# Kernel tuning notes

Measured on AMD Instinct MI355X. Metric: run time of the kernel, lower is better.

## Reference

```python
import jax, jax.numpy as jnp
import numpy as np

E_ENT = 50000   # entities
R_REL = 500     # relations (dual graph nodes)
N_EDGE = 500000 # triples
D = 256
HID = D // 2
ALPHA = 0.1
BETA = 0.3
SLOPE = 0.01    # torch F.leaky_relu default

def _leaky(x):
    return jnp.where(x > 0, x, SLOPE * x)

def _compute_r(X, head_r, tail_r):
    # mean head / tail entity embedding per relation -> [R, 2D]
    L = (head_r.T @ X) / head_r.sum(0)[:, None]
    Rm = (tail_r.T @ X) / tail_r.sum(0)[:, None]
    return jnp.concatenate([L, Rm], axis=-1)

def _dense_att(vals_in, feats, adj, w1, w2, b2, w3, b3):
    # conv1d(k=1) == linear; feats [R, 2D]
    in_fts = feats @ w1.T                # [R, HID]
    f1 = in_fts @ w2.T + b2              # [R, 1]
    f2 = in_fts @ w3.T + b3              # [R, 1]
    logits = adj * (f1 + f2.T)           # [R, R]
    bias = -1e9 * (1.0 - (adj > 0).astype(jnp.float32))
    coefs = jax.nn.softmax(_leaky(logits) + bias, axis=1)
    return jax.nn.relu(coefs @ vals_in)

def _sparse_att(X, dual_layer, row, col, rel, w, b):
    # per-relation scalar score, gathered per edge, sparse row-softmax, sparse mm
    score = (dual_layer @ w.T + b)[:, 0]          # [R]
    logit = _leaky(score[rel])                    # [E]
    m = jax.ops.segment_max(logit, row, num_segments=E_ENT)
    ex = jnp.exp(logit - m[row])
    s = jax.ops.segment_sum(ex, row, num_segments=E_ENT)
    coef = ex / s[row]
    out = jnp.zeros_like(X).at[row].add(coef[:, None] * X[col])
    return jax.nn.relu(out)

def _gcn(X, W, m_row, m_col, m_val):
    # sparse.mm(M, X * W); dropout omitted (eval mode)
    Xw = X * W
    out = jnp.zeros_like(X).at[m_row].add(m_val[:, None] * Xw[m_col])
    return jax.nn.relu(out)

def _highway(l1, l2, K, b):
    t = jax.nn.sigmoid(l1 @ K + b)
    return t * l2 + (1.0 - t) * l1

def setup_inputs() -> dict:
    key = jax.random.key(0)
    ks = jax.random.split(key, 24)
    e, r, ne, d, hid = E_ENT, R_REL, N_EDGE, D, HID
    u = lambda k, sh: jax.random.uniform(k, sh, dtype=jnp.float32)
    n = lambda k, sh: jax.random.normal(k, sh, dtype=jnp.float32)
    gl = lambda k, sh: n(k, sh) * (2.0 / (sh[0] + sh[-1])) ** 0.5
    return {
        'X0': n(ks[0], (e, d)) * 0.1,
        'head_r': u(ks[1], (e, r)),
        'tail_r': u(ks[2], (e, r)),
        'dual_A': u(ks[3], (r, r)),
        'edge_row': jax.random.randint(ks[4], (ne,), 0, e),
        'edge_col': jax.random.randint(ks[5], (ne,), 0, e),
        'edge_rel': jax.random.randint(ks[6], (ne,), 0, r),
        'm_row': jax.random.randint(ks[7], (ne,), 0, e),
        'm_col': jax.random.randint(ks[8], (ne,), 0, e),
        'm_val': u(ks[9], (ne,)) * 1e-1,
        'w_self1': gl(ks[10], (hid, 2 * d)),
        'w_self2': gl(ks[11], (1, hid)), 'b_self2': jnp.zeros((1,), jnp.float32),
        'w_self3': gl(ks[12], (1, hid)), 'b_self3': jnp.zeros((1,), jnp.float32),
        'w_sp1': gl(ks[13], (1, 2 * d)), 'b_sp1': jnp.zeros((1,), jnp.float32),
        'w_dual1': gl(ks[14], (hid, 2 * d)),
        'w_dual2': gl(ks[15], (1, hid)), 'b_dual2': jnp.zeros((1,), jnp.float32),
        'w_dual3': gl(ks[16], (1, hid)), 'b_dual3': jnp.zeros((1,), jnp.float32),
        'w_sp2': gl(ks[17], (1, 2 * d)), 'b_sp2': jnp.zeros((1,), jnp.float32),
        'w_gcn1': jnp.ones((1, d), jnp.float32),
        'w_gcn2': jnp.ones((1, d), jnp.float32),
        'k_hw1': gl(ks[18], (d, d)), 'bg_hw1': jnp.zeros((d,), jnp.float32),
        'k_hw2': gl(ks[19], (d, d)), 'bg_hw2': jnp.zeros((d,), jnp.float32),
    }

def reference(X0, head_r, tail_r, dual_A, edge_row, edge_col, edge_rel,
              m_row, m_col, m_val,
              w_self1, w_self2, b_self2, w_self3, b_self3, w_sp1, b_sp1,
              w_dual1, w_dual2, b_dual2, w_dual3, b_dual3, w_sp2, b_sp2,
              w_gcn1, w_gcn2, k_hw1, bg_hw1, k_hw2, bg_hw2):
    dX1 = _compute_r(X0, head_r, tail_r)
    dH1 = _dense_att(dX1, dX1, dual_A, w_self1, w_self2, b_self2, w_self3, b_self3)
    pH1 = _sparse_att(X0, dH1, edge_row, edge_col, edge_rel, w_sp1, b_sp1)
    pX1 = X0 + ALPHA * pH1
    dX2 = _compute_r(pX1, head_r, tail_r)
    dH2 = _dense_att(dH1, dX2, dual_A, w_dual1, w_dual2, b_dual2, w_dual3, b_dual3)
    pH2 = _sparse_att(pX1, dH2, edge_row, edge_col, edge_rel, w_sp2, b_sp2)
    pX2 = X0 + BETA * pH2
    g1 = _gcn(pX2, w_gcn1, m_row, m_col, m_val)
    h1 = _highway(pX2, g1, k_hw1, bg_hw1)
    g2 = _gcn(h1, w_gcn2, m_row, m_col, m_val)
    return _highway(h1, g2, k_hw2, bg_hw2)
```

## Files before the change

kernel.cpp:

```cpp
#include <hip/hip_runtime.h>
#include <stdint.h>

#define E_ENT 50000
#define R_REL 500
#define NEDGE 500000
#define DD 256
#define D2 512
#define KSPLIT 50
#define KCHUNK 1000

typedef unsigned short u16;
typedef unsigned int u32;
typedef __attribute__((ext_vector_type(8))) short bf16x8;
typedef __attribute__((ext_vector_type(4))) float f32x4;

__device__ __forceinline__ float bf2f(u16 u) {
  union { u32 i; float f; } v; v.i = ((u32)u) << 16; return v.f;
}
__device__ __forceinline__ u16 f2bf(float f) {
  union { float f; u32 i; } v; v.f = f;
  u32 r = v.i + 0x7fffu + ((v.i >> 16) & 1u);
  return (u16)(r >> 16);
}
__device__ __forceinline__ float lrelu(float x) { return x > 0.f ? x : 0.01f * x; }

__device__ __forceinline__ uint4 ld4g(const u16* p, bool v) {
  if (v) return *(const uint4*)p;
  return make_uint4(0u, 0u, 0u, 0u);
}

__device__ __forceinline__ int lds_addr(int col, int e) {
  return col * 64 + ((((e >> 3) ^ col ^ (col >> 3)) & 7) << 3) + (e & 7);
}

__device__ __forceinline__ void pack_store(u16* __restrict__ lds, int colBase, int e,
                                           const uint4& x, const uint4& y) {
  const u32* xp = (const u32*)&x;
  const u32* yp = (const u32*)&y;
#pragma unroll
  for (int i = 0; i < 4; ++i) {
    u32 xv = xp[i], yv = yp[i];
    u32 lo = (xv & 0xffffu) | (yv << 16);
    u32 hi = (xv >> 16) | (yv & 0xffff0000u);
    int c0 = colBase + 2 * i;
    *(u32*)(lds + lds_addr(c0, e)) = lo;
    *(u32*)(lds + lds_addr(c0 + 1, e)) = hi;
  }
}

__global__ void k_cast(const float* __restrict__ in, u16* __restrict__ out, int n4) {
  int i = blockIdx.x * 256 + threadIdx.x;
  if (i < n4) {
    float4 v = *(const float4*)(in + (size_t)i * 4);
    uint2 o;
    o.x = (u32)f2bf(v.x) | ((u32)f2bf(v.y) << 16);
    o.y = (u32)f2bf(v.z) | ((u32)f2bf(v.w) << 16);
    *(uint2*)(out + (size_t)i * 4) = o;
  }
}

__global__ __launch_bounds__(256) void k_castW(const float* __restrict__ W,
                                               u16* __restrict__ WB,
                                               float* __restrict__ sums) {
  int tid = threadIdx.x;
  int c0 = tid * 2;
  int r0 = blockIdx.x * 64;
  bool valid = c0 < R_REL;
  float s0 = 0.f, s1 = 0.f;
  for (int e = 0; e < 64; ++e) {
    int row = r0 + e;
    if (row >= E_ENT) break;
    u32 out = 0;
    if (valid) {
      float2 v = *(const float2*)(W + (size_t)row * R_REL + c0);
      s0 += v.x; s1 += v.y;
      out = (u32)f2bf(v.x) | ((u32)f2bf(v.y) << 16);
    }
    *(u32*)(WB + (size_t)row * D2 + c0) = out;
  }
  if (valid) {
    atomicAdd(&sums[c0], s0);
    atomicAdd(&sums[c0 + 1], s1);
  }
}

__global__ void k_hist(const int* __restrict__ rows, int* __restrict__ cnt) {
  int i = blockIdx.x * 256 + threadIdx.x;
  if (i < NEDGE) atomicAdd(&cnt[rows[i]], 1);
}

__global__ void k_bsum(const int* __restrict__ cnt, int* __restrict__ bsum) {
  __shared__ int sb[256];
  int t = threadIdx.x, i = blockIdx.x * 256 + t;
  sb[t] = (i < E_ENT) ? cnt[i] : 0;
  __syncthreads();
  for (int s = 128; s; s >>= 1) { if (t < s) sb[t] += sb[t + s]; __syncthreads(); }
  if (t == 0) bsum[blockIdx.x] = sb[0];
}

__global__ void k_scanb(const int* __restrict__ bsum, int* __restrict__ boff, int nb) {
  __shared__ int sb[256];
  int t = threadIdx.x;
  int v = (t < nb) ? bsum[t] : 0;
  sb[t] = v;
  __syncthreads();
  for (int o = 1; o < 256; o <<= 1) {
    int x = (t >= o) ? sb[t - o] : 0;
    __syncthreads();
    sb[t] += x;
    __syncthreads();
  }
  if (t < nb) boff[t] = sb[t] - v;
}

__global__ void k_apply(const int* __restrict__ cnt, const int* __restrict__ boff,
                        int* __restrict__ ptr, int* __restrict__ cur) {
  __shared__ int sb[256];
  int t = threadIdx.x, b = blockIdx.x, i = b * 256 + t;
  int v = (i < E_ENT) ? cnt[i] : 0;
  sb[t] = v;
  __syncthreads();
  for (int o = 1; o < 256; o <<= 1) {
    int x = (t >= o) ? sb[t - o] : 0;
    __syncthreads();
    sb[t] += x;
    __syncthreads();
  }
  if (i < E_ENT) { int ex = boff[b] + sb[t] - v; ptr[i] = ex; cur[i] = ex; }
  if (b == 0 && t == 0) ptr[E_ENT] = NEDGE;
}

__global__ void k_scat_e(const int* __restrict__ rows, const int* __restrict__ cols,
                         const int* __restrict__ rels, int* __restrict__ cur,
                         int* __restrict__ cs, int* __restrict__ rs) {
  int i = blockIdx.x * 256 + threadIdx.x;
  if (i < NEDGE) {
    int p = atomicAdd(&cur[rows[i]], 1);
    cs[p] = cols[i];
    rs[p] = rels[i];
  }
}

__global__ void k_scat_m(const int* __restrict__ rows, const int* __restrict__ cols,
                         const float* __restrict__ vals, int* __restrict__ cur,
                         int* __restrict__ cs, float* __restrict__ vs) {
  int i = blockIdx.x * 256 + threadIdx.x;
  if (i < NEDGE) {
    int p = atomicAdd(&cur[rows[i]], 1);
    cs[p] = cols[i];
    vs[p] = vals[i];
  }
}

__device__ __forceinline__ void wtx_load(const u16* __restrict__ WSel, const u16* __restrict__ XB,
                                         int eb, int e_end, int r0, int n0,
                                         int ap, int aq, int ep0, int ep1, int nq,
                                         uint4& a0, uint4& a1, uint4& b00, uint4& b01,
                                         uint4& b10, uint4& b11) {
  int ee = e_end - eb;
  const u16* p = WSel + (size_t)(eb + 2 * ap) * D2 + r0 + aq * 8;
  a0 = ld4g(p, 2 * ap < ee);
  a1 = ld4g(p + D2, 2 * ap + 1 < ee);
  const u16* q0 = XB + (size_t)(eb + 2 * ep0) * DD + n0 + nq * 8;
  b00 = ld4g(q0, 2 * ep0 < ee);
  b01 = ld4g(q0 + DD, 2 * ep0 + 1 < ee);
  const u16* q1 = XB + (size_t)(eb + 2 * ep1) * DD + n0 + nq * 8;
  b10 = ld4g(q1, 2 * ep1 < ee);
  b11 = ld4g(q1 + DD, 2 * ep1 + 1 < ee);
}

__global__ __launch_bounds__(256) void k_wtx(const u16* __restrict__ HB,
                                             const u16* __restrict__ TB,
                                             const u16* __restrict__ XB,
                                             float* __restrict__ P) {
  __shared__ __align__(16) u16 lsa2[2 * 32 * 64];
  __shared__ __align__(16) u16 lsb[128 * 64];
  const int tid = threadIdx.x;
  const int bid = blockIdx.x;
  const int swz = (bid & 7) * 200 + (bid >> 3);
  const int mtnt = swz & 31;
  const int mt = mtnt >> 1, nt = mtnt & 1;
  const int chunk = swz >> 5;
  const int r0 = mt * 32, n0 = nt * 128;
  const int lane = tid & 63, wv = tid >> 6;
  const int wm = (wv & 1) * 16, wn = (wv >> 1) * 64;
  const int l15 = lane & 15, lq = lane >> 4;
  const int ap = (tid & 127) >> 2, aq = tid & 3;
  const int ep0 = tid >> 4, nq = tid & 15;
  const int ep1 = ep0 + 16;
  const u16* WSel = (tid < 128) ? HB : TB;
  u16* lsaSel = lsa2 + (tid >> 7) * (32 * 64);
  const int e_begin = chunk * KCHUNK;
  const int e_end = min(e_begin + KCHUNK, E_ENT);
  const int iters = (e_end - e_begin + 63) >> 6;

  f32x4 accH[4], accT[4];
#pragma unroll
  for (int t = 0; t < 4; ++t) { accH[t] = (f32x4)0.f; accT[t] = (f32x4)0.f; }

  uint4 a0, a1, b00, b01, b10, b11;
  wtx_load(WSel, XB, e_begin, e_end, r0, n0, ap, aq, ep0, ep1, nq, a0, a1, b00, b01, b10, b11);

  int eb = e_begin;
  for (int it = 0; it < iters; ++it) {
    __syncthreads();
    pack_store(lsaSel, aq * 8, 2 * ap, a0, a1);
    pack_store(lsb, nq * 8, 2 * ep0, b00, b01);
    pack_store(lsb, nq * 8, 2 * ep1, b10, b11);
    __syncthreads();
    eb += 64;
    if (it + 1 < iters)
      wtx_load(WSel, XB, eb, e_end, r0, n0, ap, aq, ep0, ep1, nq, a0, a1, b00, b01, b10, b11);
#pragma unroll
    for (int ks = 0; ks < 2; ++ks) {
      bf16x8 afH = *(const bf16x8*)(lsa2 + lds_addr(wm + l15, ks * 32 + lq * 8));
      bf16x8 afT = *(const bf16x8*)(lsa2 + 32 * 64 + lds_addr(wm + l15, ks * 32 + lq * 8));
#pragma unroll
      for (int t = 0; t < 4; ++t) {
        bf16x8 bv = *(const bf16x8*)(lsb + lds_addr(wn + t * 16 + l15, ks * 32 + lq * 8));
        accH[t] = __builtin_amdgcn_mfma_f32_16x16x32_bf16(afH, bv, accH[t], 0, 0, 0);
        accT[t] = __builtin_amdgcn_mfma_f32_16x16x32_bf16(afT, bv, accT[t], 0, 0, 0);
      }
    }
  }
#pragma unroll
  for (int t = 0; t < 4; ++t) {
#pragma unroll
    for (int rg = 0; rg < 4; ++rg) {
      int row = r0 + wm + lq * 4 + rg;
      if (row < R_REL) {
        int col = n0 + wn + t * 16 + l15;
        atomicAdd(&P[row * D2 + col], accH[t][rg]);
        atomicAdd(&P[row * D2 + col + 256], accT[t][rg]);
      }
    }
  }
}

__global__ void k_fin(float* __restrict__ P, const float* __restrict__ hsum,
                      const float* __restrict__ tsum) {
  int i = blockIdx.x * 256 + threadIdx.x;
  if (i < R_REL * D2) {
    int r = i >> 9, c = i & 511;
    P[i] = P[i] / (c < 256 ? hsum[r] : tsum[r]);
  }
}

__global__ __launch_bounds__(128) void k_infts(const float* __restrict__ feats,
                                               const float* __restrict__ w1,
                                               const float* __restrict__ w2, const float* __restrict__ b2,
                                               const float* __restrict__ w3, const float* __restrict__ b3,
                                               float* __restrict__ f1, float* __restrict__ f2) {
  __shared__ float fl[512];
  __shared__ float red[128];
  int r = blockIdx.x, t = threadIdx.x;
  for (int i = t; i < 512; i += 128) fl[i] = feats[r * 512 + i];
  __syncthreads();
  float a = 0.f;
  const float* wrow = w1 + (size_t)t * 512;
  for (int k = 0; k < 512; k += 4) {
    float4 v = *(const float4*)(wrow + k);
    a += fl[k + 0] * v.x + fl[k + 1] * v.y + fl[k + 2] * v.z + fl[k + 3] * v.w;
  }
  red[t] = a * w2[t];
  __syncthreads();
  for (int s = 64; s; s >>= 1) { if (t < s) red[t] += red[t + s]; __syncthreads(); }
  if (t == 0) f1[r] = red[0] + b2[0];
  __syncthreads();
  red[t] = a * w3[t];
  __syncthreads();
  for (int s = 64; s; s >>= 1) { if (t < s) red[t] += red[t + s]; __syncthreads(); }
  if (t == 0) f2[r] = red[0] + b3[0];
}

__global__ __launch_bounds__(256) void k_att(const float* __restrict__ adj,
                                             const float* __restrict__ f1,
                                             const float* __restrict__ f2,
                                             const float* __restrict__ vals,
                                             float* __restrict__ dH) {
  __shared__ float coef[512];
  __shared__ float red[256];
  int r = blockIdx.x, t = threadIdx.x;
  float f1r = f1[r];
  float z0, z1 = -1e30f;
  {
    float a = adj[r * 500 + t];
    float z = lrelu(a * (f1r + f2[t]));
    if (!(a > 0.f)) z += -1e9f;
    z0 = z;
  }
  int c1 = t + 256;
  if (c1 < 500) {
    float a = adj[r * 500 + c1];
    float z = lrelu(a * (f1r + f2[c1]));
    if (!(a > 0.f)) z += -1e9f;
    z1 = z;
  }
  red[t] = fmaxf(z0, z1);
  __syncthreads();
  for (int s = 128; s; s >>= 1) { if (t < s) red[t] = fmaxf(red[t], red[t + s]); __syncthreads(); }
  float m = red[0];
  __syncthreads();
  float e0 = expf(z0 - m);
  float e1 = (c1 < 500) ? expf(z1 - m) : 0.f;
  coef[t] = e0;
  coef[c1] = e1;
  red[t] = e0 + e1;
  __syncthreads();
  for (int s = 128; s; s >>= 1) { if (t < s) red[t] += red[t + s]; __syncthreads(); }
  float inv = 1.f / red[0];
  float accA = 0.f, accB = 0.f;
  int dA = t, dB = t + 256;
  for (int c = 0; c < 500; ++c) {
    float cf = coef[c];
    accA += cf * vals[c * 512 + dA];
    accB += cf * vals[c * 512 + dB];
  }
  dH[r * 512 + dA] = fmaxf(accA * inv, 0.f);
  dH[r * 512 + dB] = fmaxf(accB * inv, 0.f);
}

__global__ void k_score(const float* __restrict__ dH, const float* __restrict__ w,
                        const float* __restrict__ b, float* __restrict__ score) {
  int r = blockIdx.x, lane = threadIdx.x;
  float a = 0.f;
  for (int k = lane; k < 512; k += 64) a += dH[r * 512 + k] * w[k];
  for (int o = 32; o; o >>= 1) a += __shfl_xor(a, o, 64);
  if (lane == 0) score[r] = a + b[0];
}

__global__ void k_els(const float* __restrict__ score, float* __restrict__ EL) {
  __shared__ float red[512];
  int t = threadIdx.x;
  float v = (t < R_REL) ? lrelu(score[t]) : -3.0e38f;
  red[t] = v;
  __syncthreads();
  for (int s = 256; s; s >>= 1) { if (t < s) red[t] = fmaxf(red[t], red[t + s]); __syncthreads(); }
  float m = red[0];
  EL[t] = (t < R_REL) ? expf(v - m) : 0.f;
}

__global__ __launch_bounds__(256) void k_spatt(const u16* __restrict__ src,
                                               const float* __restrict__ base,
                                               const int* __restrict__ ptr,
                                               const int* __restrict__ cols,
                                               const int* __restrict__ rels,
                                               const float* __restrict__ EL, float alpha,
                                               u16* __restrict__ outb, float* __restrict__ outf) {
  __shared__ float sEL[512];
  const int tid = threadIdx.x;
  sEL[tid] = EL[tid];
  sEL[tid + 256] = EL[tid + 256];
  __syncthreads();
  const int lane = tid & 63;
  const int e = blockIdx.x * 4 + (tid >> 6);
  int p0 = ptr[e], p1 = ptr[e + 1];
  float a0 = 0.f, a1 = 0.f, a2 = 0.f, a3 = 0.f;
  if (p1 > p0) {
    float s = 0.f;
    for (int j = p0 + lane; j < p1; j += 64) s += sEL[rels[j]];
    for (int o = 32; o; o >>= 1) s += __shfl_xor(s, o, 64);
    float inv = 1.f / s;
    for (int jb = p0; jb < p1; jb += 64) {
      int n = min(64, p1 - jb);
      int cl = 0; float wl = 0.f;
      if (lane < n) { cl = cols[jb + lane]; wl = sEL[rels[jb + lane]] * inv; }
      int jj = 0;
      for (; jj + 4 <= n; jj += 4) {
        int c0 = __shfl(cl, jj), c1 = __shfl(cl, jj + 1), c2 = __shfl(cl, jj + 2), c3 = __shfl(cl, jj + 3);
        float w0 = __shfl(wl, jj), w1 = __shfl(wl, jj + 1), w2 = __shfl(wl, jj + 2), w3 = __shfl(wl, jj + 3);
        uint2 v0 = *(const uint2*)(src + (size_t)c0 * DD + lane * 4);
        uint2 v1 = *(const uint2*)(src + (size_t)c1 * DD + lane * 4);
        uint2 v2 = *(const uint2*)(src + (size_t)c2 * DD + lane * 4);
        uint2 v3 = *(const uint2*)(src + (size_t)c3 * DD + lane * 4);
        a0 += w0 * bf2f((u16)(v0.x & 0xffffu)) + w1 * bf2f((u16)(v1.x & 0xffffu))
            + w2 * bf2f((u16)(v2.x & 0xffffu)) + w3 * bf2f((u16)(v3.x & 0xffffu));
        a1 += w0 * bf2f((u16)(v0.x >> 16)) + w1 * bf2f((u16)(v1.x >> 16))
            + w2 * bf2f((u16)(v2.x >> 16)) + w3 * bf2f((u16)(v3.x >> 16));
        a2 += w0 * bf2f((u16)(v0.y & 0xffffu)) + w1 * bf2f((u16)(v1.y & 0xffffu))
            + w2 * bf2f((u16)(v2.y & 0xffffu)) + w3 * bf2f((u16)(v3.y & 0xffffu));
        a3 += w0 * bf2f((u16)(v0.y >> 16)) + w1 * bf2f((u16)(v1.y >> 16))
            + w2 * bf2f((u16)(v2.y >> 16)) + w3 * bf2f((u16)(v3.y >> 16));
      }
      for (; jj < n; ++jj) {
        int c = __shfl(cl, jj);
        float w = __shfl(wl, jj);
        uint2 v = *(const uint2*)(src + (size_t)c * DD + lane * 4);
        a0 += w * bf2f((u16)(v.x & 0xffffu));
        a1 += w * bf2f((u16)(v.x >> 16));
        a2 += w * bf2f((u16)(v.y & 0xffffu));
        a3 += w * bf2f((u16)(v.y >> 16));
      }
    }
  }
  size_t off = (size_t)e * DD + lane * 4;
  float4 bv = *(const float4*)(base + off);
  float o0 = bv.x + alpha * fmaxf(a0, 0.f);
  float o1 = bv.y + alpha * fmaxf(a1, 0.f);
  float o2 = bv.z + alpha * fmaxf(a2, 0.f);
  float o3 = bv.w + alpha * fmaxf(a3, 0.f);
  uint2 ov;
  ov.x = (u32)f2bf(o0) | ((u32)f2bf(o1) << 16);
  ov.y = (u32)f2bf(o2) | ((u32)f2bf(o3) << 16);
  *(uint2*)(outb + off) = ov;
  if (outf) *(float4*)(outf + off) = make_float4(o0, o1, o2, o3);
}

__global__ __launch_bounds__(256) void k_gcn(const u16* __restrict__ src,
                                             const int* __restrict__ ptr,
                                             const int* __restrict__ cols,
                                             const float* __restrict__ vals,
                                             const float* __restrict__ wg,
                                             float* __restrict__ gout) {
  const int lane = threadIdx.x & 63;
  const int e = blockIdx.x * 4 + (threadIdx.x >> 6);
  int p0 = ptr[e], p1 = ptr[e + 1];
  float a0 = 0.f, a1 = 0.f, a2 = 0.f, a3 = 0.f;
  for (int jb = p0; jb < p1; jb += 64) {
    int n = min(64, p1 - jb);
    int cl = 0; float wl = 0.f;
    if (lane < n) { cl = cols[jb + lane]; wl = vals[jb + lane]; }
    int jj = 0;
    for (; jj + 4 <= n; jj += 4) {
      int c0 = __shfl(cl, jj), c1 = __shfl(cl, jj + 1), c2 = __shfl(cl, jj + 2), c3 = __shfl(cl, jj + 3);
      float w0 = __shfl(wl, jj), w1 = __shfl(wl, jj + 1), w2 = __shfl(wl, jj + 2), w3 = __shfl(wl, jj + 3);
      uint2 v0 = *(const uint2*)(src + (size_t)c0 * DD + lane * 4);
      uint2 v1 = *(const uint2*)(src + (size_t)c1 * DD + lane * 4);
      uint2 v2 = *(const uint2*)(src + (size_t)c2 * DD + lane * 4);
      uint2 v3 = *(const uint2*)(src + (size_t)c3 * DD + lane * 4);
      a0 += w0 * bf2f((u16)(v0.x & 0xffffu)) + w1 * bf2f((u16)(v1.x & 0xffffu))
          + w2 * bf2f((u16)(v2.x & 0xffffu)) + w3 * bf2f((u16)(v3.x & 0xffffu));
      a1 += w0 * bf2f((u16)(v0.x >> 16)) + w1 * bf2f((u16)(v1.x >> 16))
          + w2 * bf2f((u16)(v2.x >> 16)) + w3 * bf2f((u16)(v3.x >> 16));
      a2 += w0 * bf2f((u16)(v0.y & 0xffffu)) + w1 * bf2f((u16)(v1.y & 0xffffu))
          + w2 * bf2f((u16)(v2.y & 0xffffu)) + w3 * bf2f((u16)(v3.y & 0xffffu));
      a3 += w0 * bf2f((u16)(v0.y >> 16)) + w1 * bf2f((u16)(v1.y >> 16))
          + w2 * bf2f((u16)(v2.y >> 16)) + w3 * bf2f((u16)(v3.y >> 16));
    }
    for (; jj < n; ++jj) {
      int c = __shfl(cl, jj);
      float w = __shfl(wl, jj);
      uint2 v = *(const uint2*)(src + (size_t)c * DD + lane * 4);
      a0 += w * bf2f((u16)(v.x & 0xffffu));
      a1 += w * bf2f((u16)(v.x >> 16));
      a2 += w * bf2f((u16)(v.y & 0xffffu));
      a3 += w * bf2f((u16)(v.y >> 16));
    }
  }
  int d = lane * 4;
  float4 wv = *(const float4*)(wg + d);
  float4 o = make_float4(fmaxf(a0 * wv.x, 0.f), fmaxf(a1 * wv.y, 0.f),
                         fmaxf(a2 * wv.z, 0.f), fmaxf(a3 * wv.w, 0.f));
  *(float4*)(gout + (size_t)e * DD + d) = o;
}

__global__ __launch_bounds__(256) void k_hw(const u16* __restrict__ xb,
                                            const float* __restrict__ xf,
                                            const float* __restrict__ g,
                                            const u16* __restrict__ KB,
                                            const float* __restrict__ bg,
                                            float* __restrict__ outf,
                                            u16* __restrict__ outb) {
  __shared__ __align__(16) u16 la[64 * 64];
  __shared__ __align__(16) u16 lb[64 * 64];
  const int tid = threadIdx.x;
  const int bid = blockIdx.x;
  const int swz = (bid & 7) * 391 + (bid >> 3);
  const int e0 = (swz >> 2) * 64;
  const int n0 = (swz & 3) * 64;
  const int lane = tid & 63, wv = tid >> 6;
  const int m0 = wv * 16;
  const int l15 = lane & 15, lq = lane >> 4;
  const int am = tid >> 3, aoct = tid & 7;
  const int kp = tid >> 3, nq8 = tid & 7;
  f32x4 acc[4];
#pragma unroll
  for (int t = 0; t < 4; ++t) acc[t] = (f32x4)0.f;

  for (int kc = 0; kc < 4; ++kc) {
    {
      const u16* pa = xb + (size_t)(e0 + am) * DD + kc * 64 + aoct * 8;
      uint4 va = ld4g(pa, e0 + am < E_ENT);
      *(uint4*)(la + lds_addr(am, aoct * 8)) = va;
      const u16* pa2 = xb + (size_t)(e0 + am + 32) * DD + kc * 64 + aoct * 8;
      uint4 va2 = ld4g(pa2, e0 + am + 32 < E_ENT);
      *(uint4*)(la + lds_addr(am + 32, aoct * 8)) = va2;
      const u16* pb = KB + (size_t)(kc * 64 + 2 * kp) * DD + n0 + nq8 * 8;
      uint4 xk = *(const uint4*)pb;
      uint4 yk = *(const uint4*)(pb + DD);
      pack_store(lb, nq8 * 8, 2 * kp, xk, yk);
    }
    __syncthreads();
#pragma unroll
    for (int ks = 0; ks < 2; ++ks) {
      bf16x8 af = *(const bf16x8*)(la + lds_addr(m0 + l15, ks * 32 + lq * 8));
#pragma unroll
      for (int t = 0; t < 4; ++t) {
        bf16x8 bv = *(const bf16x8*)(lb + lds_addr(t * 16 + l15, ks * 32 + lq * 8));
        acc[t] = __builtin_amdgcn_mfma_f32_16x16x32_bf16(af, bv, acc[t], 0, 0, 0);
      }
    }
    __syncthreads();
  }
#pragma unroll
  for (int t = 0; t < 4; ++t) {
    int col = n0 + t * 16 + l15;
    float bgv = bg[col];
#pragma unroll
    for (int rg = 0; rg < 4; ++rg) {
      int row = e0 + m0 + lq * 4 + rg;
      if (row < E_ENT) {
        float z = acc[t][rg] + bgv;
        float tt = 1.f / (1.f + expf(-z));
        size_t off = (size_t)row * DD + col;
        float hv = tt * g[off] + (1.f - tt) * xf[off];
        outf[off] = hv;
        if (outb) outb[off] = f2bf(hv);
      }
    }
  }
}

extern "C" void kernel_launch(void* const* d_in, const int* in_sizes, int n_in,
                              void* d_out, int out_size, void* d_ws, size_t ws_size,
                              hipStream_t stream) {
  (void)in_sizes; (void)n_in; (void)out_size;
  const float* X0 = (const float*)d_in[0];
  const float* head = (const float*)d_in[1];
  const float* tail = (const float*)d_in[2];
  const float* adj = (const float*)d_in[3];
  const int* erow = (const int*)d_in[4];
  const int* ecol = (const int*)d_in[5];
  const int* erel = (const int*)d_in[6];
  const int* mrow = (const int*)d_in[7];
  const int* mcol = (const int*)d_in[8];
  const float* mval = (const float*)d_in[9];
  const float* w_self1 = (const float*)d_in[10];
  const float* w_self2 = (const float*)d_in[11];
  const float* b_self2 = (const float*)d_in[12];
  const float* w_self3 = (const float*)d_in[13];
  const float* b_self3 = (const float*)d_in[14];
  const float* w_sp1 = (const float*)d_in[15];
  const float* b_sp1 = (const float*)d_in[16];
  const float* w_dual1 = (const float*)d_in[17];
  const float* w_dual2 = (const float*)d_in[18];
  const float* b_dual2 = (const float*)d_in[19];
  const float* w_dual3 = (const float*)d_in[20];
  const float* b_dual3 = (const float*)d_in[21];
  const float* w_sp2 = (const float*)d_in[22];
  const float* b_sp2 = (const float*)d_in[23];
  const float* w_gcn1 = (const float*)d_in[24];
  const float* w_gcn2 = (const float*)d_in[25];
  const float* k_hw1 = (const float*)d_in[26];
  const float* bg_hw1 = (const float*)d_in[27];
  const float* k_hw2 = (const float*)d_in[28];
  const float* bg_hw2 = (const float*)d_in[29];

  char* ws = (char*)d_ws;
  size_t o = 0;
  auto take = [&](size_t bytes) -> char* {
    o = (o + 255) & ~(size_t)255;
    char* p = ws + o;
    o += bytes;
    return p;
  };
  u16* X0B  = (u16*)take((size_t)E_ENT * DD * 2);
  u16* PX1B = (u16*)take((size_t)E_ENT * DD * 2);
  u16* PX2B = (u16*)take((size_t)E_ENT * DD * 2);
  u16* H1B  = (u16*)take((size_t)E_ENT * DD * 2);
  float* PX2F = (float*)take((size_t)E_ENT * DD * 4);
  float* G    = (float*)take((size_t)E_ENT * DD * 4);
  float* P1   = (float*)take((size_t)512 * 512 * 4);
  float* P2   = (float*)take((size_t)512 * 512 * 4);
  float* DH1  = (float*)take((size_t)512 * 512 * 4);
  float* DH2  = (float*)take((size_t)512 * 512 * 4);
  float* HS   = (float*)take(1024 * 4);
  float* F1   = (float*)take(512 * 4);
  float* F2   = (float*)take(512 * 4);
  float* SCORE = (float*)take(512 * 4);
  float* EL   = (float*)take(512 * 4);
  u16* KB1 = (u16*)take((size_t)DD * DD * 2);
  u16* KB2 = (u16*)take((size_t)DD * DD * 2);
  int* BSUM = (int*)take(256 * 4);
  int* BOFF = (int*)take(256 * 4);
  int* EPTR = (int*)take((size_t)(E_ENT + 1) * 4);
  int* ECUR = (int*)take((size_t)(E_ENT + 1) * 4);
  int* ECOLS = (int*)take((size_t)NEDGE * 4);
  int* ERELS = (int*)take((size_t)NEDGE * 4);
  int* MPTR = (int*)take((size_t)(E_ENT + 1) * 4);
  int* MCUR = (int*)take((size_t)(E_ENT + 1) * 4);
  int* MCOLS = (int*)take((size_t)NEDGE * 4);
  float* MVALS = (float*)take((size_t)NEDGE * 4);

  u16* HB = (u16*)PX2F;
  u16* TB = (u16*)G;

  if (o > ws_size) {
    hipMemsetAsync(d_out, 0, (size_t)E_ENT * DD * 4, stream);
    return;
  }

  hipMemsetAsync(P1, 0, (size_t)512 * 512 * 4, stream);
  hipMemsetAsync(P2, 0, (size_t)512 * 512 * 4, stream);
  hipMemsetAsync(HS, 0, 1024 * 4, stream);
  hipMemsetAsync(ECUR, 0, (size_t)(E_ENT + 1) * 4, stream);
  hipMemsetAsync(MCUR, 0, (size_t)(E_ENT + 1) * 4, stream);

  const int GE = (NEDGE + 255) / 256;
  const int GB = (E_ENT + 255) / 256;
  const int GW = (E_ENT + 63) / 64;

  k_cast<<<(E_ENT * DD / 4 + 255) / 256, 256, 0, stream>>>(X0, X0B, E_ENT * DD / 4);
  k_cast<<<64, 256, 0, stream>>>(k_hw1, KB1, DD * DD / 4);
  k_cast<<<64, 256, 0, stream>>>(k_hw2, KB2, DD * DD / 4);
  k_castW<<<GW, 256, 0, stream>>>(head, HB, HS);
  k_castW<<<GW, 256, 0, stream>>>(tail, TB, HS + 512);

  k_hist<<<GE, 256, 0, stream>>>(erow, ECUR);
  k_bsum<<<GB, 256, 0, stream>>>(ECUR, BSUM);
  k_scanb<<<1, 256, 0, stream>>>(BSUM, BOFF, GB);
  k_apply<<<GB, 256, 0, stream>>>(ECUR, BOFF, EPTR, ECUR);
  k_scat_e<<<GE, 256, 0, stream>>>(erow, ecol, erel, ECUR, ECOLS, ERELS);
  k_hist<<<GE, 256, 0, stream>>>(mrow, MCUR);
  k_bsum<<<GB, 256, 0, stream>>>(MCUR, BSUM);
  k_scanb<<<1, 256, 0, stream>>>(BSUM, BOFF, GB);
  k_apply<<<GB, 256, 0, stream>>>(MCUR, BOFF, MPTR, MCUR);
  k_scat_m<<<GE, 256, 0, stream>>>(mrow, mcol, mval, MCUR, MCOLS, MVALS);

  k_wtx<<<32 * KSPLIT, 256, 0, stream>>>(HB, TB, X0B, P1);
  k_fin<<<1000, 256, 0, stream>>>(P1, HS, HS + 512);
  k_infts<<<500, 128, 0, stream>>>(P1, w_self1, w_self2, b_self2, w_self3, b_self3, F1, F2);
  k_att<<<500, 256, 0, stream>>>(adj, F1, F2, P1, DH1);
  k_score<<<500, 64, 0, stream>>>(DH1, w_sp1, b_sp1, SCORE);
  k_els<<<1, 512, 0, stream>>>(SCORE, EL);
  k_spatt<<<12500, 256, 0, stream>>>(X0B, X0, EPTR, ECOLS, ERELS, EL, 0.1f, PX1B, nullptr);

  k_wtx<<<32 * KSPLIT, 256, 0, stream>>>(HB, TB, PX1B, P2);
  k_fin<<<1000, 256, 0, stream>>>(P2, HS, HS + 512);
  k_infts<<<500, 128, 0, stream>>>(P2, w_dual1, w_dual2, b_dual2, w_dual3, b_dual3, F1, F2);
  k_att<<<500, 256, 0, stream>>>(adj, F1, F2, DH1, DH2);
  k_score<<<500, 64, 0, stream>>>(DH2, w_sp2, b_sp2, SCORE);
  k_els<<<1, 512, 0, stream>>>(SCORE, EL);
  k_spatt<<<12500, 256, 0, stream>>>(PX1B, X0, EPTR, ECOLS, ERELS, EL, 0.3f, PX2B, PX2F);

  k_gcn<<<12500, 256, 0, stream>>>(PX2B, MPTR, MCOLS, MVALS, w_gcn1, G);
  k_hw<<<782 * 4, 256, 0, stream>>>(PX2B, PX2F, G, KB1, bg_hw1, PX2F, H1B);
  k_gcn<<<12500, 256, 0, stream>>>(H1B, MPTR, MCOLS, MVALS, w_gcn2, G);
  k_hw<<<782 * 4, 256, 0, stream>>>(H1B, PX2F, G, KB2, bg_hw2, (float*)d_out, nullptr);
}
```

Baseline: 1.109 ms.

## Fuse head/tail fp32-to-bf16 cast and column sums into WtX GEMM loads

Drops the separate k_castW pre-pass that converted the head/tail incidence matrices to padded bf16 and summed their columns. k_wtx now loads fp32 rows directly, packs them to bf16 in registers before the LDS store, and on the first call also accumulates the per-relation column sums, reduced through LDS and then atomics. This removes a full read-write pass over two large matrices and two launches. The cost is that each GEMM call now reads fp32 data, twice the bytes of bf16, and each slice is fetched by both n-tiles, so total traffic may not shrink unless the cache absorbs the repeats.

```diff
diff --git a/kernel.cpp b/kernel.cpp
--- a/kernel.cpp
+++ b/kernel.cpp
@@ -27,6 +27,19 @@
 __device__ __forceinline__ uint4 ld4g(const u16* p, bool v) {
   if (v) return *(const uint4*)p;
   return make_uint4(0u, 0u, 0u, 0u);
+}
+__device__ __forceinline__ float4 ldf4(const float* p, bool v) {
+  if (v) return *(const float4*)p;
+  return make_float4(0.f, 0.f, 0.f, 0.f);
+}
+
+__device__ __forceinline__ uint4 pk4(const float4& x, const float4& y) {
+  uint4 r;
+  r.x = (u32)f2bf(x.x) | ((u32)f2bf(x.y) << 16);
+  r.y = (u32)f2bf(x.z) | ((u32)f2bf(x.w) << 16);
+  r.z = (u32)f2bf(y.x) | ((u32)f2bf(y.y) << 16);
+  r.w = (u32)f2bf(y.z) | ((u32)f2bf(y.w) << 16);
+  return r;
 }
 
 __device__ __forceinline__ int lds_addr(int col, int e) {
@@ -59,31 +72,6 @@
   }
 }
 
-__global__ __launch_bounds__(256) void k_castW(const float* __restrict__ W,
-                                               u16* __restrict__ WB,
-                                               float* __restrict__ sums) {
-  int tid = threadIdx.x;
-  int c0 = tid * 2;
-  int r0 = blockIdx.x * 64;
-  bool valid = c0 < R_REL;
-  float s0 = 0.f, s1 = 0.f;
-  for (int e = 0; e < 64; ++e) {
-    int row = r0 + e;
-    if (row >= E_ENT) break;
-    u32 out = 0;
-    if (valid) {
-      float2 v = *(const float2*)(W + (size_t)row * R_REL + c0);
-      s0 += v.x; s1 += v.y;
-      out = (u32)f2bf(v.x) | ((u32)f2bf(v.y) << 16);
-    }
-    *(u32*)(WB + (size_t)row * D2 + c0) = out;
-  }
-  if (valid) {
-    atomicAdd(&sums[c0], s0);
-    atomicAdd(&sums[c0 + 1], s1);
-  }
-}
-
 __global__ void k_hist(const int* __restrict__ rows, int* __restrict__ cnt) {
   int i = blockIdx.x * 256 + threadIdx.x;
   if (i < NEDGE) atomicAdd(&cnt[rows[i]], 1);
@@ -152,15 +140,20 @@
   }
 }
 
-__device__ __forceinline__ void wtx_load(const u16* __restrict__ WSel, const u16* __restrict__ XB,
+__device__ __forceinline__ void wtx_load(const float* __restrict__ WSel, const u16* __restrict__ XB,
                                          int eb, int e_end, int r0, int n0,
                                          int ap, int aq, int ep0, int ep1, int nq,
-                                         uint4& a0, uint4& a1, uint4& b00, uint4& b01,
-                                         uint4& b10, uint4& b11) {
+                                         float4& f00, float4& f01, float4& f10, float4& f11,
+                                         uint4& b00, uint4& b01, uint4& b10, uint4& b11) {
   int ee = e_end - eb;
-  const u16* p = WSel + (size_t)(eb + 2 * ap) * D2 + r0 + aq * 8;
-  a0 = ld4g(p, 2 * ap < ee);
-  a1 = ld4g(p + D2, 2 * ap + 1 < ee);
+  int c0 = r0 + aq * 8;
+  bool cv0 = c0 < R_REL, cv1 = (c0 + 4) < R_REL;
+  bool r0ok = 2 * ap < ee, r1ok = 2 * ap + 1 < ee;
+  const float* p = WSel + (size_t)(eb + 2 * ap) * R_REL + c0;
+  f00 = ldf4(p, r0ok && cv0);
+  f01 = ldf4(p + 4, r0ok && cv1);
+  f10 = ldf4(p + R_REL, r1ok && cv0);
+  f11 = ldf4(p + R_REL + 4, r1ok && cv1);
   const u16* q0 = XB + (size_t)(eb + 2 * ep0) * DD + n0 + nq * 8;
   b00 = ld4g(q0, 2 * ep0 < ee);
   b01 = ld4g(q0 + DD, 2 * ep0 + 1 < ee);
@@ -169,10 +162,11 @@
   b11 = ld4g(q1 + DD, 2 * ep1 + 1 < ee);
 }
 
-__global__ __launch_bounds__(256) void k_wtx(const u16* __restrict__ HB,
-                                             const u16* __restrict__ TB,
+__global__ __launch_bounds__(256) void k_wtx(const float* __restrict__ HW,
+                                             const float* __restrict__ TW,
                                              const u16* __restrict__ XB,
-                                             float* __restrict__ P) {
+                                             float* __restrict__ P,
+                                             float* __restrict__ sums) {
   __shared__ __align__(16) u16 lsa2[2 * 32 * 64];
   __shared__ __align__(16) u16 lsb[128 * 64];
   const int tid = threadIdx.x;
@@ -188,8 +182,9 @@
   const int ap = (tid & 127) >> 2, aq = tid & 3;
   const int ep0 = tid >> 4, nq = tid & 15;
   const int ep1 = ep0 + 16;
-  const u16* WSel = (tid < 128) ? HB : TB;
+  const float* WSel = (tid < 128) ? HW : TW;
   u16* lsaSel = lsa2 + (tid >> 7) * (32 * 64);
+  const bool dosum = (sums != nullptr) && (nt == 0);
   const int e_begin = chunk * KCHUNK;
   const int e_end = min(e_begin + KCHUNK, E_ENT);
   const int iters = (e_end - e_begin + 63) >> 6;
@@ -197,20 +192,29 @@
   f32x4 accH[4], accT[4];
 #pragma unroll
   for (int t = 0; t < 4; ++t) { accH[t] = (f32x4)0.f; accT[t] = (f32x4)0.f; }
-
-  uint4 a0, a1, b00, b01, b10, b11;
-  wtx_load(WSel, XB, e_begin, e_end, r0, n0, ap, aq, ep0, ep1, nq, a0, a1, b00, b01, b10, b11);
+  float s0 = 0.f, s1 = 0.f, s2 = 0.f, s3 = 0.f, s4 = 0.f, s5 = 0.f, s6 = 0.f, s7 = 0.f;
+
+  float4 f00, f01, f10, f11;
+  uint4 b00, b01, b10, b11;
+  wtx_load(WSel, XB, e_begin, e_end, r0, n0, ap, aq, ep0, ep1, nq,
+           f00, f01, f10, f11, b00, b01, b10, b11);
 
   int eb = e_begin;
   for (int it = 0; it < iters; ++it) {
     __syncthreads();
+    uint4 a0 = pk4(f00, f01), a1 = pk4(f10, f11);
+    if (dosum) {
+      s0 += f00.x + f10.x; s1 += f00.y + f10.y; s2 += f00.z + f10.z; s3 += f00.w + f10.w;
+      s4 += f01.x + f11.x; s5 += f01.y + f11.y; s6 += f01.z + f11.z; s7 += f01.w + f11.w;
+    }
     pack_store(lsaSel, aq * 8, 2 * ap, a0, a1);
     pack_store(lsb, nq * 8, 2 * ep0, b00, b01);
     pack_store(lsb, nq * 8, 2 * ep1, b10, b11);
     __syncthreads();
     eb += 64;
     if (it + 1 < iters)
-      wtx_load(WSel, XB, eb, e_end, r0, n0, ap, aq, ep0, ep1, nq, a0, a1, b00, b01, b10, b11);
+      wtx_load(WSel, XB, eb, e_end, r0, n0, ap, aq, ep0, ep1, nq,
+               f00, f01, f10, f11, b00, b01, b10, b11);
 #pragma unroll
     for (int ks = 0; ks < 2; ++ks) {
       bf16x8 afH = *(const bf16x8*)(lsa2 + lds_addr(wm + l15, ks * 32 + lq * 8));
@@ -223,6 +227,25 @@
       }
     }
   }
+
+  if (dosum) {
+    __syncthreads();
+    float* scr = (float*)lsb;
+    int half = tid >> 7;
+    int base = half * 1024 + aq * 256 + ap;
+    scr[base + 0 * 32] = s0; scr[base + 1 * 32] = s1;
+    scr[base + 2 * 32] = s2; scr[base + 3 * 32] = s3;
+    scr[base + 4 * 32] = s4; scr[base + 5 * 32] = s5;
+    scr[base + 6 * 32] = s6; scr[base + 7 * 32] = s7;
+    __syncthreads();
+    if (tid < 64) {
+      int hh = tid >> 5, aq2 = (tid >> 3) & 3, j = tid & 7;
+      float v = 0.f;
+      for (int a = 0; a < 32; ++a) v += scr[hh * 1024 + aq2 * 256 + j * 32 + a];
+      atomicAdd(&sums[hh * 512 + r0 + aq2 * 8 + j], v);
+    }
+  }
+
 #pragma unroll
   for (int t = 0; t < 4; ++t) {
 #pragma unroll
@@ -592,9 +615,6 @@
   int* MCOLS = (int*)take((size_t)NEDGE * 4);
   float* MVALS = (float*)take((size_t)NEDGE * 4);
 
-  u16* HB = (u16*)PX2F;
-  u16* TB = (u16*)G;
-
   if (o > ws_size) {
     hipMemsetAsync(d_out, 0, (size_t)E_ENT * DD * 4, stream);
     return;
@@ -608,13 +628,10 @@
 
   const int GE = (NEDGE + 255) / 256;
   const int GB = (E_ENT + 255) / 256;
-  const int GW = (E_ENT + 63) / 64;
 
   k_cast<<<(E_ENT * DD / 4 + 255) / 256, 256, 0, stream>>>(X0, X0B, E_ENT * DD / 4);
   k_cast<<<64, 256, 0, stream>>>(k_hw1, KB1, DD * DD / 4);
   k_cast<<<64, 256, 0, stream>>>(k_hw2, KB2, DD * DD / 4);
-  k_castW<<<GW, 256, 0, stream>>>(head, HB, HS);
-  k_castW<<<GW, 256, 0, stream>>>(tail, TB, HS + 512);
 
   k_hist<<<GE, 256, 0, stream>>>(erow, ECUR);
   k_bsum<<<GB, 256, 0, stream>>>(ECUR, BSUM);
@@ -627,7 +644,7 @@
   k_apply<<<GB, 256, 0, stream>>>(MCUR, BOFF, MPTR, MCUR);
   k_scat_m<<<GE, 256, 0, stream>>>(mrow, mcol, mval, MCUR, MCOLS, MVALS);
 
-  k_wtx<<<32 * KSPLIT, 256, 0, stream>>>(HB, TB, X0B, P1);
+  k_wtx<<<32 * KSPLIT, 256, 0, stream>>>(head, tail, X0B, P1, HS);
   k_fin<<<1000, 256, 0, stream>>>(P1, HS, HS + 512);
   k_infts<<<500, 128, 0, stream>>>(P1, w_self1, w_self2, b_self2, w_self3, b_self3, F1, F2);
   k_att<<<500, 256, 0, stream>>>(adj, F1, F2, P1, DH1);
@@ -635,7 +652,7 @@
   k_els<<<1, 512, 0, stream>>>(SCORE, EL);
   k_spatt<<<12500, 256, 0, stream>>>(X0B, X0, EPTR, ECOLS, ERELS, EL, 0.1f, PX1B, nullptr);
 
-  k_wtx<<<32 * KSPLIT, 256, 0, stream>>>(HB, TB, PX1B, P2);
+  k_wtx<<<32 * KSPLIT, 256, 0, stream>>>(head, tail, PX1B, P2, nullptr);
   k_fin<<<1000, 256, 0, stream>>>(P2, HS, HS + 512);
   k_infts<<<500, 128, 0, stream>>>(P2, w_dual1, w_dual2, b_dual2, w_dual3, b_dual3, F1, F2);
   k_att<<<500, 256, 0, stream>>>(adj, F1, F2, DH1, DH2);
```

Measured after the change: 1.011 ms. 8.8% less time.
